# Kernel tuning notes

Measured on AMD Instinct MI355X. Metric: run time of the kernel, lower is better.

## Reference

```python
import jax, jax.numpy as jnp
import numpy as np

N_NODES = 50000


def _gcn_norm(edge_index, num_nodes):
    # PyG GCNConv default: add self-loops, symmetric normalization D^-1/2 A D^-1/2
    row, col = edge_index[0], edge_index[1]
    loop = jnp.arange(num_nodes, dtype=edge_index.dtype)
    row = jnp.concatenate([row, loop])
    col = jnp.concatenate([col, loop])
    deg = jax.ops.segment_sum(jnp.ones_like(col, dtype=jnp.float32), col,
                              num_segments=num_nodes)
    deg_inv_sqrt = jnp.where(deg > 0, jax.lax.rsqrt(deg), 0.0)
    norm = deg_inv_sqrt[row] * deg_inv_sqrt[col]  # [E + N]
    return row, col, norm


def _gcn_conv(x, row, col, norm, W, b):
    h = x @ W                                   # [N, out]
    msg = h[row] * norm[:, None]                # gather + scale, [E+N, out]
    out = jax.ops.segment_sum(msg, col, num_segments=x.shape[0])  # scatter-add
    return out + b


def setup_inputs() -> dict:
    key = jax.random.key(0)
    k_x, k_e, k_w1, k_w2 = jax.random.split(key, 4)
    n, e, d = N_NODES, 800000, 64
    x = jax.random.normal(k_x, (n, d), dtype=jnp.float32)
    edge_index = jax.random.randint(k_e, (2, e), 0, n, dtype=jnp.int64)
    # Glorot init like PyG's Linear inside GCNConv (bias separate, zero-init here as randn-small)
    s1 = (6.0 / (d + d)) ** 0.5
    W1 = jax.random.uniform(k_w1, (d, d), jnp.float32, -s1, s1)
    W2 = jax.random.uniform(k_w2, (d, d), jnp.float32, -s1, s1)
    b1 = jnp.zeros((d,), jnp.float32)
    b2 = jnp.zeros((d,), jnp.float32)
    return {"x": x, "edge_index": edge_index, "W1": W1, "b1": b1, "W2": W2, "b2": b2}


def reference(x, edge_index, W1, b1, W2, b2):
    row, col, norm = _gcn_norm(edge_index, x.shape[0])
    h = _gcn_conv(x, row, col, norm, W1, b1)   # layer 1: in -> out
    h = _gcn_conv(h, row, col, norm, W2, b2)   # layer 2: out -> out
    return h
```

## Files before the change

kernel.cpp:

```cpp
#include <hip/hip_runtime.h>
#include <hip/hip_fp16.h>

#define DD 64
#define BSH 6
#define BNODES 64
#define NSUB 8
#define SCAP 256
#define BCAP 1536
#define TSH 14

__global__ __launch_bounds__(256) void k_zero(int4* __restrict__ p, int n4) {
    int i = blockIdx.x * 256 + threadIdx.x;
    if (i < n4) p[i] = make_int4(0, 0, 0, 0);
}

__global__ __launch_bounds__(256) void k_fill3(const int* __restrict__ rowi,
                                               const int* __restrict__ coli,
                                               int* __restrict__ cur,
                                               unsigned int* __restrict__ pk, int E) {
    int i = blockIdx.x * 256 + threadIdx.x;
    if (i < E) {
        int c = coli[i];
        int idx = (c >> BSH) * NSUB + (blockIdx.x & (NSUB - 1));
        int p = atomicAdd(&cur[idx * 16], 1);
        if (p < SCAP)
            pk[(size_t)idx * SCAP + p] =
                (unsigned int)rowi[i] | ((unsigned int)(c & (BNODES - 1)) << 16);
    }
}

__global__ __launch_bounds__(256) void k_bsortmm(const int* __restrict__ cur,
                                                 const unsigned int* __restrict__ pk,
                                                 int* __restrict__ off_s,
                                                 int* __restrict__ off_e,
                                                 float* __restrict__ dis,
                                                 int* __restrict__ srt,
                                                 const float* __restrict__ X,
                                                 const float* __restrict__ W,
                                                 __half* __restrict__ H, int n) {
    __shared__ unsigned int stage[NSUB * SCAP];
    __shared__ float xs[BNODES * 65];
    __shared__ int cnt[256];
    __shared__ int cbase[256];
    __shared__ int sb[NSUB + 1];
    __shared__ int wsum[4];
    __shared__ float sdis[BNODES];
    const int t = threadIdx.x;
    const int b = blockIdx.x;
    const int c0 = b * BNODES;

    cnt[t] = 0;
    if (t < NSUB) {
        int v = cur[(b * NSUB + t) * 16];
        if (v > SCAP) v = SCAP;
        int x = v;
#pragma unroll
        for (int d = 1; d < NSUB; d <<= 1) {
            int u = __shfl_up(x, d, NSUB);
            if ((t & (NSUB - 1)) >= d) x += u;
        }
        sb[t + 1] = x;
        if (t == 0) sb[0] = 0;
    }
    __syncthreads();
    int tot = sb[NSUB];

#pragma unroll
    for (int s = 0; s < NSUB; ++s) {
        int q0 = sb[s], len = sb[s + 1] - q0;
        const unsigned int* src = pk + ((size_t)b * NSUB + s) * SCAP;
        for (int i = t; i < len; i += 256) stage[q0 + i] = src[i];
    }
    {
        const float4* X4 = (const float4*)X;
        for (int idx = t; idx < BNODES * 16; idx += 256) {
            int row = idx >> 4, q = idx & 15, c = c0 + row;
            float4 v = make_float4(0.f, 0.f, 0.f, 0.f);
            if (c < n) v = X4[(size_t)c * 16 + q];
            int base = row * 65 + q * 4;
            xs[base + 0] = v.x; xs[base + 1] = v.y;
            xs[base + 2] = v.z; xs[base + 3] = v.w;
        }
    }
    __syncthreads();

    for (int i = t; i < tot; i += 256) {
        unsigned int k = stage[i];
        int key = (int)((k >> 16) << 2) | (int)((k & 0xFFFFu) >> TSH);
        atomicAdd(&cnt[key], 1);
    }
    __syncthreads();

    {
        const int lane = t & 63, w = t >> 6;
        int v = cnt[t], s = v;
#pragma unroll
        for (int d = 1; d < 64; d <<= 1) {
            int u = __shfl_up(s, d);
            if (lane >= d) s += u;
        }
        if (lane == 63) wsum[w] = s;
        __syncthreads();
        if (t == 0) {
            int a = 0;
#pragma unroll
            for (int q = 0; q < 4; ++q) { int tmp = wsum[q]; wsum[q] = a; a += tmp; }
        }
        __syncthreads();
        cbase[t] = wsum[w] + s - v;
    }
    __syncthreads();

    if (t < BNODES) {
        int st  = cbase[t << 2];
        int deg = cnt[(t << 2)] + cnt[(t << 2) | 1] + cnt[(t << 2) | 2] + cnt[(t << 2) | 3];
        float dv = rsqrtf((float)(deg + 1));
        sdis[t] = dv;
        int c = c0 + t;
        if (c < n) {
            off_s[c] = b * BCAP + st;
            off_e[c] = b * BCAP + st + deg;
            dis[c] = dv;
        }
    }
    __syncthreads();

    int sbeg = b * BCAP;
    for (int i = t; i < tot; i += 256) {
        unsigned int k = stage[i];
        int key = (int)((k >> 16) << 2) | (int)((k & 0xFFFFu) >> TSH);
        int pos = atomicAdd(&cbase[key], 1);
        srt[sbeg + pos] = (int)(k & 0xFFFFu);
    }
    __syncthreads();

    const int lane  = t & 63;
    const int jbase = __builtin_amdgcn_readfirstlane((t >> 6) * 16);
    float acc[16];
#pragma unroll
    for (int j = 0; j < 16; ++j) acc[j] = 0.f;
#pragma unroll 1
    for (int kc = 0; kc < 16; ++kc) {
#pragma unroll
        for (int u = 0; u < 4; ++u) {
            float sk = xs[lane * 65 + kc * 4 + u];
            const float* Wk = W + (kc * 4 + u) * 64 + jbase;
#pragma unroll
            for (int j = 0; j < 16; ++j)
                acc[j] = fmaf(sk, Wk[j], acc[j]);
        }
    }
    int c = c0 + lane;
    if (c < n) {
        float d = sdis[lane];
        __half2 hh[8];
#pragma unroll
        for (int q = 0; q < 8; ++q)
            hh[q] = __floats2half2_rn(acc[2 * q] * d, acc[2 * q + 1] * d);
        uint4* dst = (uint4*)(H + (size_t)c * DD + jbase);
        const uint4* src = (const uint4*)hh;
        dst[0] = src[0];
        dst[1] = src[1];
    }
}

__global__ __launch_bounds__(64) void k_mm_h(const __half* __restrict__ Xh,
                                             const float* __restrict__ W,
                                             const float* __restrict__ dis,
                                             __half* __restrict__ H, int n) {
    int lane  = threadIdx.x;
    int tile  = blockIdx.x >> 1;
    int jbase = (blockIdx.x & 1) * 32;
    int r     = tile * 64 + lane;
    int rc    = min(r, n - 1);

    const uint4* X8 = (const uint4*)Xh;
    float acc[32];
#pragma unroll
    for (int j = 0; j < 32; ++j) acc[j] = 0.f;

#pragma unroll 1
    for (int kc = 0; kc < 8; ++kc) {
        uint4 hv = X8[(size_t)rc * 8 + kc];
        float xk[8];
        const __half2* hp = (const __half2*)&hv;
#pragma unroll
        for (int q = 0; q < 4; ++q) {
            float2 f = __half22float2(hp[q]);
            xk[2 * q] = f.x; xk[2 * q + 1] = f.y;
        }
#pragma unroll
        for (int u = 0; u < 8; ++u) {
            const float* Wk = W + (kc * 8 + u) * 64 + jbase;
#pragma unroll
            for (int j = 0; j < 32; ++j)
                acc[j] = fmaf(xk[u], Wk[j], acc[j]);
        }
    }
    if (r < n) {
        float d = dis[r];
        __half2 hh[16];
#pragma unroll
        for (int q = 0; q < 16; ++q)
            hh[q] = __floats2half2_rn(acc[2 * q] * d, acc[2 * q + 1] * d);
        uint4* dst = (uint4*)(H + (size_t)r * DD + jbase);
        const uint4* src = (const uint4*)hh;
#pragma unroll
        for (int q = 0; q < 4; ++q) dst[q] = src[q];
    }
}

template<int HOUT>
__global__ __launch_bounds__(256) void k_agg(const int* __restrict__ off_s,
                                             const int* __restrict__ off_e,
                                             const int* __restrict__ srt,
                                             const float* __restrict__ dis,
                                             const __half* __restrict__ hs,
                                             const float* __restrict__ bias,
                                             float* __restrict__ outf,
                                             __half* __restrict__ outh, int n) {
    int lane = threadIdx.x & 63;
    int j    = lane & 31;
    int hsel = lane >> 5;
    int c = __builtin_amdgcn_readfirstlane(blockIdx.x * 4 + (threadIdx.x >> 6));
    if (c >= n) return;

    int s = __builtin_amdgcn_readfirstlane(off_s[c]);
    int e = __builtin_amdgcn_readfirstlane(off_e[c]);

    const __half2* hs2 = (const __half2*)hs;

    float ax = 0.f, ay = 0.f;
    if (hsel == 0) {
        float2 f = __half22float2(hs2[(size_t)c * 32 + j]);
        ax = f.x; ay = f.y;
    }
    int p = s;
    for (; p + 8 <= e; p += 8) {
        int r0 = srt[p + 0], r1 = srt[p + 1], r2 = srt[p + 2], r3 = srt[p + 3];
        int r4 = srt[p + 4], r5 = srt[p + 5], r6 = srt[p + 6], r7 = srt[p + 7];
        int ra = hsel ? r1 : r0;
        int rb = hsel ? r3 : r2;
        int rg = hsel ? r5 : r4;
        int rd = hsel ? r7 : r6;
        float2 f0 = __half22float2(hs2[(size_t)ra * 32 + j]);
        float2 f1 = __half22float2(hs2[(size_t)rb * 32 + j]);
        float2 f2 = __half22float2(hs2[(size_t)rg * 32 + j]);
        float2 f3 = __half22float2(hs2[(size_t)rd * 32 + j]);
        ax += (f0.x + f1.x) + (f2.x + f3.x);
        ay += (f0.y + f1.y) + (f2.y + f3.y);
    }
    for (; p + 2 <= e; p += 2) {
        int r0 = srt[p], r1 = srt[p + 1];
        int ra = hsel ? r1 : r0;
        float2 f = __half22float2(hs2[(size_t)ra * 32 + j]);
        ax += f.x; ay += f.y;
    }
    if (p < e && hsel == 0) {
        float2 f = __half22float2(hs2[(size_t)srt[p] * 32 + j]);
        ax += f.x; ay += f.y;
    }
    ax += __shfl_xor(ax, 32);
    ay += __shfl_xor(ay, 32);
    if (hsel == 0) {
        float d = dis[c];
        float2 bb = ((const float2*)bias)[j];
        float ox = bb.x + d * ax;
        float oy = bb.y + d * ay;
        if (HOUT)
            ((__half2*)outh)[(size_t)c * 32 + j] = __floats2half2_rn(ox, oy);
        else
            ((float2*)outf)[(size_t)c * 32 + j] = make_float2(ox, oy);
    }
}

extern "C" void kernel_launch(void* const* d_in, const int* in_sizes, int n_in,
                              void* d_out, int out_size, void* d_ws, size_t ws_size,
                              hipStream_t stream) {
    const float* x  = (const float*)d_in[0];
    const int*   ei = (const int*)d_in[1];
    const float* W1 = (const float*)d_in[2];
    const float* b1 = (const float*)d_in[3];
    const float* W2 = (const float*)d_in[4];
    const float* b2 = (const float*)d_in[5];
    float* out = (float*)d_out;

    int n = in_sizes[0] / DD;
    int E = in_sizes[1] / 2;
    const int* rowi = ei;
    const int* coli = ei + E;
    int nb = (n + BNODES - 1) / BNODES;
    int M  = nb * NSUB;

    char* ws = (char*)d_ws;
    int*          cur   = (int*)ws;
    int*          off_s = (int*)(ws + (size_t)1024 * 1024);
    int*          off_e = (int*)(ws + (size_t)1280 * 1024);
    float*        dis   = (float*)(ws + (size_t)1536 * 1024);
    unsigned int* pk    = (unsigned int*)(ws + (size_t)2048 * 1024);
    int*          srt   = (int*)(ws + (size_t)9216 * 1024);
    __half*       hs    = (__half*)(ws + (size_t)14336 * 1024);
    __half*       o1h   = (__half*)(ws + (size_t)21504 * 1024);

    int n4    = M * 4;
    int nb_z  = (n4 + 255) / 256;
    int nb_e  = (E + 255) / 256;
    int nb_mm = ((n + 63) / 64) * 2;
    int nb_ag = (n + 3) / 4;

    k_zero   <<<nb_z, 256, 0, stream>>>((int4*)cur, n4);
    k_fill3  <<<nb_e, 256, 0, stream>>>(rowi, coli, cur, pk, E);
    k_bsortmm<<<nb, 256, 0, stream>>>(cur, pk, off_s, off_e, dis, srt, x, W1, hs, n);

    k_agg<1><<<nb_ag, 256, 0, stream>>>(off_s, off_e, srt, dis, hs, b1,
                                        (float*)nullptr, o1h, n);

    k_mm_h  <<<nb_mm, 64, 0, stream>>>(o1h, W2, dis, hs, n);
    k_agg<0><<<nb_ag, 256, 0, stream>>>(off_s, off_e, srt, dis, hs, b2,
                                        out, (__half*)nullptr, n);
}
```

Before: 129.1 us.

## Fuse layer-1 aggregation with layer-2 matmul in one kernel

Replaces the separate layer-1 aggregation kernel and the half-precision matmul kernel with one fused kernel. Each wave aggregates one node's neighbors, stages the row in shared memory, and multiplies it by W2, which each block first loads into LDS. This removes one launch and the write/read round trip of the intermediate half-precision buffer, and keeps the layer-1 output in fp32 before the matmul. In exchange, every block reloads 16KB of W2 and the per-node matvec adds 64 LDS reads per lane per node.

```diff
diff --git a/kernel.cpp b/kernel.cpp
--- a/kernel.cpp
+++ b/kernel.cpp
@@ -164,61 +164,93 @@
     }
 }
 
-__global__ __launch_bounds__(64) void k_mm_h(const __half* __restrict__ Xh,
-                                             const float* __restrict__ W,
-                                             const float* __restrict__ dis,
-                                             __half* __restrict__ H, int n) {
-    int lane  = threadIdx.x;
-    int tile  = blockIdx.x >> 1;
-    int jbase = (blockIdx.x & 1) * 32;
-    int r     = tile * 64 + lane;
-    int rc    = min(r, n - 1);
-
-    const uint4* X8 = (const uint4*)Xh;
-    float acc[32];
-#pragma unroll
-    for (int j = 0; j < 32; ++j) acc[j] = 0.f;
-
-#pragma unroll 1
-    for (int kc = 0; kc < 8; ++kc) {
-        uint4 hv = X8[(size_t)rc * 8 + kc];
-        float xk[8];
-        const __half2* hp = (const __half2*)&hv;
-#pragma unroll
-        for (int q = 0; q < 4; ++q) {
-            float2 f = __half22float2(hp[q]);
-            xk[2 * q] = f.x; xk[2 * q + 1] = f.y;
-        }
-#pragma unroll
-        for (int u = 0; u < 8; ++u) {
-            const float* Wk = W + (kc * 8 + u) * 64 + jbase;
-#pragma unroll
-            for (int j = 0; j < 32; ++j)
-                acc[j] = fmaf(xk[u], Wk[j], acc[j]);
-        }
-    }
-    if (r < n) {
-        float d = dis[r];
-        __half2 hh[16];
-#pragma unroll
-        for (int q = 0; q < 16; ++q)
-            hh[q] = __floats2half2_rn(acc[2 * q] * d, acc[2 * q + 1] * d);
-        uint4* dst = (uint4*)(H + (size_t)r * DD + jbase);
-        const uint4* src = (const uint4*)hh;
-#pragma unroll
-        for (int q = 0; q < 4; ++q) dst[q] = src[q];
-    }
-}
-
-template<int HOUT>
+__global__ __launch_bounds__(256) void k_aggmm(const int* __restrict__ off_s,
+                                               const int* __restrict__ off_e,
+                                               const int* __restrict__ srt,
+                                               const float* __restrict__ dis,
+                                               const __half* __restrict__ hs,
+                                               const float* __restrict__ bias1,
+                                               const float* __restrict__ W2,
+                                               __half* __restrict__ hs2, int n) {
+    __shared__ float wld[4096];
+    __shared__ float srow[4][72];
+    const int t = threadIdx.x;
+
+    {
+        const float4* W4 = (const float4*)W2;
+        float4* wl4 = (float4*)wld;
+#pragma unroll
+        for (int q = 0; q < 4; ++q) wl4[t + 256 * q] = W4[t + 256 * q];
+    }
+    __syncthreads();
+
+    const int lane = t & 63;
+    const int wv   = t >> 6;
+    const int j    = lane & 31;
+    const int hsel = lane >> 5;
+    int c = __builtin_amdgcn_readfirstlane(blockIdx.x * 4 + wv);
+    if (c >= n) return;
+
+    int s = __builtin_amdgcn_readfirstlane(off_s[c]);
+    int e = __builtin_amdgcn_readfirstlane(off_e[c]);
+    float d = dis[c];
+
+    const __half2* hs2v = (const __half2*)hs;
+
+    float ax = 0.f, ay = 0.f;
+    if (hsel == 0) {
+        float2 f = __half22float2(hs2v[(size_t)c * 32 + j]);
+        ax = f.x; ay = f.y;
+    }
+    int p = s;
+    for (; p + 8 <= e; p += 8) {
+        int r0 = srt[p + 0], r1 = srt[p + 1], r2 = srt[p + 2], r3 = srt[p + 3];
+        int r4 = srt[p + 4], r5 = srt[p + 5], r6 = srt[p + 6], r7 = srt[p + 7];
+        int ra = hsel ? r1 : r0;
+        int rb = hsel ? r3 : r2;
+        int rg = hsel ? r5 : r4;
+        int rd = hsel ? r7 : r6;
+        float2 f0 = __half22float2(hs2v[(size_t)ra * 32 + j]);
+        float2 f1 = __half22float2(hs2v[(size_t)rb * 32 + j]);
+        float2 f2 = __half22float2(hs2v[(size_t)rg * 32 + j]);
+        float2 f3 = __half22float2(hs2v[(size_t)rd * 32 + j]);
+        ax += (f0.x + f1.x) + (f2.x + f3.x);
+        ay += (f0.y + f1.y) + (f2.y + f3.y);
+    }
+    for (; p + 2 <= e; p += 2) {
+        int r0 = srt[p], r1 = srt[p + 1];
+        int ra = hsel ? r1 : r0;
+        float2 f = __half22float2(hs2v[(size_t)ra * 32 + j]);
+        ax += f.x; ay += f.y;
+    }
+    if (p < e && hsel == 0) {
+        float2 f = __half22float2(hs2v[(size_t)srt[p] * 32 + j]);
+        ax += f.x; ay += f.y;
+    }
+    ax += __shfl_xor(ax, 32);
+    ay += __shfl_xor(ay, 32);
+
+    if (hsel == 0) {
+        float2 bb = ((const float2*)bias1)[j];
+        srow[wv][2 * j]     = bb.x + d * ax;
+        srow[wv][2 * j + 1] = bb.y + d * ay;
+    }
+    __builtin_amdgcn_wave_barrier();
+
+    float acc = 0.f;
+#pragma unroll 8
+    for (int k = 0; k < 64; ++k)
+        acc = fmaf(srow[wv][k], wld[k * 64 + lane], acc);
+    hs2[(size_t)c * DD + lane] = __float2half(d * acc);
+}
+
 __global__ __launch_bounds__(256) void k_agg(const int* __restrict__ off_s,
                                              const int* __restrict__ off_e,
                                              const int* __restrict__ srt,
                                              const float* __restrict__ dis,
                                              const __half* __restrict__ hs,
                                              const float* __restrict__ bias,
-                                             float* __restrict__ outf,
-                                             __half* __restrict__ outh, int n) {
+                                             float* __restrict__ outf, int n) {
     int lane = threadIdx.x & 63;
     int j    = lane & 31;
     int hsel = lane >> 5;
@@ -265,12 +297,7 @@
     if (hsel == 0) {
         float d = dis[c];
         float2 bb = ((const float2*)bias)[j];
-        float ox = bb.x + d * ax;
-        float oy = bb.y + d * ay;
-        if (HOUT)
-            ((__half2*)outh)[(size_t)c * 32 + j] = __floats2half2_rn(ox, oy);
-        else
-            ((float2*)outf)[(size_t)c * 32 + j] = make_float2(ox, oy);
+        ((float2*)outf)[(size_t)c * 32 + j] = make_float2(bb.x + d * ax, bb.y + d * ay);
     }
 }
 
@@ -299,23 +326,19 @@
     float*        dis   = (float*)(ws + (size_t)1536 * 1024);
     unsigned int* pk    = (unsigned int*)(ws + (size_t)2048 * 1024);
     int*          srt   = (int*)(ws + (size_t)9216 * 1024);
-    __half*       hs    = (__half*)(ws + (size_t)14336 * 1024);
-    __half*       o1h   = (__half*)(ws + (size_t)21504 * 1024);
+    __half*       hs1   = (__half*)(ws + (size_t)14336 * 1024);
+    __half*       hs2   = (__half*)(ws + (size_t)21504 * 1024);
 
     int n4    = M * 4;
     int nb_z  = (n4 + 255) / 256;
     int nb_e  = (E + 255) / 256;
-    int nb_mm = ((n + 63) / 64) * 2;
     int nb_ag = (n + 3) / 4;
 
     k_zero   <<<nb_z, 256, 0, stream>>>((int4*)cur, n4);
     k_fill3  <<<nb_e, 256, 0, stream>>>(rowi, coli, cur, pk, E);
-    k_bsortmm<<<nb, 256, 0, stream>>>(cur, pk, off_s, off_e, dis, srt, x, W1, hs, n);
-
-    k_agg<1><<<nb_ag, 256, 0, stream>>>(off_s, off_e, srt, dis, hs, b1,
-                                        (float*)nullptr, o1h, n);
-
-    k_mm_h  <<<nb_mm, 64, 0, stream>>>(o1h, W2, dis, hs, n);
-    k_agg<0><<<nb_ag, 256, 0, stream>>>(off_s, off_e, srt, dis, hs, b2,
-                                        out, (__half*)nullptr, n);
-}
+    k_bsortmm<<<nb, 256, 0, stream>>>(cur, pk, off_s, off_e, dis, srt, x, W1, hs1, n);
+
+    k_aggmm<<<nb_ag, 256, 0, stream>>>(off_s, off_e, srt, dis, hs1, b1, W2, hs2, n);
+
+    k_agg<<<nb_ag, 256, 0, stream>>>(off_s, off_e, srt, dis, hs2, b2, out, n);
+}
```

Measured after the change: 121.3 us. -6.0%, faster.
